# Performance work log

Measured on AMD Instinct MI355X. Metric: run time of the kernel, lower is better.

Reference implementation:

```python
import jax, jax.numpy as jnp
import numpy as np

N, E, R = 50000, 500000, 3
IN, HID, OUT = 128, 128, 128
NEG_SLOPE = 0.2


def setup_inputs() -> dict:
    key = jax.random.key(0)
    ks = jax.random.split(key, 16)
    g = lambda i, shape: jax.random.normal(ks[i], shape, jnp.float32) * 0.1
    return {
        "x": jax.random.normal(ks[0], (N, IN), jnp.float32),
        "edge_index": jax.random.randint(ks[1], (2, E), 0, N, jnp.int32),
        "edge_type": jax.random.randint(ks[2], (E,), 0, R, jnp.int32),
        "edge_attr": jax.random.normal(ks[3], (E, 1), jnp.float32),
        # conv1 params (RGATConv: per-relation weight, q/k/e attention vectors, edge lin, bias)
        "w1": g(4, (R, IN, HID)), "q1": g(5, (HID, 1)), "k1": g(6, (HID, 1)),
        "le1": g(7, (1, HID)), "e1": g(8, (HID, 1)), "b1": jnp.zeros((HID,), jnp.float32),
        # conv2 params
        "w2": g(9, (R, HID, OUT)), "q2": g(10, (OUT, 1)), "k2": g(11, (OUT, 1)),
        "le2": g(12, (1, OUT)), "e2": g(13, (OUT, 1)), "b2": jnp.zeros((OUT,), jnp.float32),
    }


def _rgat_conv(x, src, dst, edge_type, edge_attr, w, q, k, le, e, b):
    """PyG RGATConv: heads=1, dim=1, additive-self-attention, across-relation softmax."""
    n = x.shape[0]
    # Per-relation linear at node level (equiv. to per-edge bmm with w[edge_type])
    xw = jnp.einsum('ni,rio->rno', x, w)            # [R, N, C]
    x_j = xw[edge_type, src]                          # [E, C] transformed source feats
    x_i = xw[edge_type, dst]                          # [E, C] transformed target feats
    # additive attention logits: q(x_i) + k(x_j) + e(lin_edge(edge_attr))
    alpha = x_i @ q + x_j @ k + (edge_attr @ le) @ e  # [E, 1]
    alpha = jax.nn.leaky_relu(alpha, negative_slope=NEG_SLOPE)
    # across-relation softmax over incoming edges of each target node
    amax = jax.ops.segment_max(alpha, dst, num_segments=n)
    amax = jnp.where(jnp.isfinite(amax), amax, 0.0)   # empty segments -> 0
    ex = jnp.exp(alpha - amax[dst])
    denom = jax.ops.segment_sum(ex, dst, num_segments=n)
    alpha = ex / (denom[dst] + 1e-16)
    # weighted scatter-add aggregation, then bias (concat=True, heads=1)
    out = jax.ops.segment_sum(alpha * x_j, dst, num_segments=n)  # [N, C]
    return out + b


def reference(x, edge_index, edge_type, edge_attr,
              w1, q1, k1, le1, e1, b1,
              w2, q2, k2, le2, e2, b2):
    src, dst = edge_index[0], edge_index[1]
    h = jax.nn.relu(_rgat_conv(x, src, dst, edge_type, edge_attr, w1, q1, k1, le1, e1, b1))
    return _rgat_conv(h, src, dst, edge_type, edge_attr, w2, q2, k2, le2, e2, b2)
```

## Files before the change

kernel.cpp:

```cpp
#include <hip/hip_runtime.h>
#include <hip/hip_bf16.h>
#include <math.h>

typedef __bf16 bf16x8 __attribute__((ext_vector_type(8)));
typedef float f32x4 __attribute__((ext_vector_type(4)));

#define CDIM 128

__global__ void sentinel_kernel(float* outf) {
  if (threadIdx.x == 0) outf[0] = 12345.0f;
}

__global__ __launch_bounds__(256) void prep_hist_kernel(
    const float* __restrict__ w1, const float* __restrict__ w2,
    __hip_bfloat16* __restrict__ wt,
    const float* __restrict__ le1, const float* __restrict__ e1,
    const float* __restrict__ le2, const float* __restrict__ e2,
    float* __restrict__ outc, const int* __restrict__ dstv,
    int* __restrict__ deg, int perW, int E) {
  const int b = blockIdx.x;
  const int tid = threadIdx.x;
  if (b < 48) {
    int t = b * 256 + tid;
    if (t >= perW * 2) return;
    const float* w = (t < perW) ? w1 : w2;
    int tt = (t < perW) ? t : t - perW;
    int r = tt >> 11;
    int rem = tt & 2047;
    int kb = rem >> 7;
    int o = rem & 127;
    const float* wr = w + ((size_t)r << 14);
    union { __hip_bfloat16 h[8]; int4 v; } u;
#pragma unroll
    for (int j = 0; j < 8; ++j)
      u.h[j] = __float2bfloat16(wr[(size_t)(kb * 8 + j) * CDIM + o]);
    *reinterpret_cast<int4*>(wt + (size_t)t * 8) = u.v;
  } else if (b == 48) {
    if (tid < 64) {
      float v1 = le1[tid] * e1[tid] + le1[tid + 64] * e1[tid + 64];
      float v2 = le2[tid] * e2[tid] + le2[tid + 64] * e2[tid + 64];
#pragma unroll
      for (int off = 32; off > 0; off >>= 1) {
        v1 += __shfl_xor(v1, off, 64);
        v2 += __shfl_xor(v2, off, 64);
      }
      if (tid == 0) { outc[0] = v1; outc[1] = v2; }
    }
  } else {
    int e0 = (b - 49) * 1024 + tid * 4;
    if (e0 + 3 < E) {
      int4 d4 = *reinterpret_cast<const int4*>(&dstv[e0]);
      atomicAdd(&deg[d4.x], 1);
      atomicAdd(&deg[d4.y], 1);
      atomicAdd(&deg[d4.z], 1);
      atomicAdd(&deg[d4.w], 1);
    } else {
      for (int t = 0; t < 4; ++t) {
        int e = e0 + t;
        if (e < E) atomicAdd(&deg[dstv[e]], 1);
      }
    }
  }
}


__global__ __launch_bounds__(256) void scan1_kernel(const int* __restrict__ deg,
                                                    int* __restrict__ rowptr,
                                                    int* __restrict__ partials, int n) {
  __shared__ int sh[256];
  int t = threadIdx.x;
  int base = blockIdx.x * 1024;
  int idx = base + t * 4;
  int v[4]; int s = 0;
#pragma unroll
  for (int j = 0; j < 4; ++j) { v[j] = (idx + j < n) ? deg[idx + j] : 0; s += v[j]; }
  sh[t] = s;
  __syncthreads();
  for (int off = 1; off < 256; off <<= 1) {
    int x = (t >= off) ? sh[t - off] : 0;
    __syncthreads();
    sh[t] += x;
    __syncthreads();
  }
  int excl = sh[t] - s;
  if (t == 255) partials[blockIdx.x] = sh[255];
  int run = excl;
#pragma unroll
  for (int j = 0; j < 4; ++j) {
    if (idx + j < n) rowptr[idx + j] = run;
    run += v[j];
  }
}

__global__ __launch_bounds__(256) void scan3_kernel(int* __restrict__ rowptr,
                                                    int* __restrict__ cursor,
                                                    const int* __restrict__ partials,
                                                    int nb, int n, int E) {
  __shared__ int spfx[64];
  int t = threadIdx.x;
  if (t < 64) {
    int pv = (t < nb) ? partials[t] : 0;
    int v = pv;
#pragma unroll
    for (int off = 1; off < 64; off <<= 1) {
      int u = __shfl_up(v, off, 64);
      if (t >= off) v += u;
    }
    spfx[t] = v - pv;
  }
  __syncthreads();
  int i = blockIdx.x * 256 + t;
  if (i < n) {
    int v = rowptr[i] + spfx[i >> 10];
    rowptr[i] = v;
    cursor[i] = v;
  } else if (i == n) {
    rowptr[n] = E;
  }
}

__global__ __launch_bounds__(256) void scatter_kernel(
    const int* __restrict__ srcv, const int* __restrict__ dstv,
    const int* __restrict__ etype, const float* __restrict__ eattr,
    int* __restrict__ cursor, int2* __restrict__ kattr, int E, int n) {
  int e0 = blockIdx.x * 1024 + threadIdx.x * 4;
  if (e0 + 3 < E) {
    int4 s4 = *reinterpret_cast<const int4*>(&srcv[e0]);
    int4 d4 = *reinterpret_cast<const int4*>(&dstv[e0]);
    int4 t4 = *reinterpret_cast<const int4*>(&etype[e0]);
    float4 a4 = *reinterpret_cast<const float4*>(&eattr[e0]);
    int p0 = atomicAdd(&cursor[d4.x], 1);
    kattr[p0] = make_int2(t4.x * n + s4.x, __float_as_int(a4.x));
    int p1 = atomicAdd(&cursor[d4.y], 1);
    kattr[p1] = make_int2(t4.y * n + s4.y, __float_as_int(a4.y));
    int p2 = atomicAdd(&cursor[d4.z], 1);
    kattr[p2] = make_int2(t4.z * n + s4.z, __float_as_int(a4.z));
    int p3 = atomicAdd(&cursor[d4.w], 1);
    kattr[p3] = make_int2(t4.w * n + s4.w, __float_as_int(a4.w));
  } else {
    for (int t = 0; t < 4; ++t) {
      int e = e0 + t;
      if (e < E) {
        int p = atomicAdd(&cursor[dstv[e]], 1);
        kattr[p] = make_int2(etype[e] * n + srcv[e], __float_as_int(eattr[e]));
      }
    }
  }
}

template <int BF16IN>
__device__ __forceinline__ void gemm_body64(
    int tb, const float* __restrict__ xf, const __hip_bfloat16* __restrict__ xb,
    const __hip_bfloat16* __restrict__ wt,
    const float* __restrict__ qv, const float* __restrict__ kv,
    __hip_bfloat16* __restrict__ xwout, float* __restrict__ sq,
    float* __restrict__ sk, int n, __hip_bfloat16* wlds, float* qls, float* kls) {
  const int tid = threadIdx.x;
  const int wave = tid >> 6, lane = tid & 63;
  const int quad = lane >> 4, c16 = lane & 15;
  const int m = tb * 64 + wave * 16 + c16;
  const bool ok = m < n;

  if (tid < 128) qls[tid] = qv[tid];
  else kls[tid - 128] = kv[tid - 128];

  bf16x8 zf;
#pragma unroll
  for (int j = 0; j < 8; ++j) zf[j] = (__bf16)0.0f;

  bf16x8 af[4];
#pragma unroll
  for (int ks = 0; ks < 4; ++ks) {
    if (ok) {
      if (BF16IN) {
        af[ks] = *reinterpret_cast<const bf16x8*>(
            xb + (size_t)m * CDIM + ks * 32 + quad * 8);
      } else {
        const float* xp = xf + (size_t)m * CDIM + ks * 32 + quad * 8;
        f32x4 x0 = *reinterpret_cast<const f32x4*>(xp);
        f32x4 x1 = *reinterpret_cast<const f32x4*>(xp + 4);
        bf16x8 a;
#pragma unroll
        for (int j = 0; j < 4; ++j) { a[j] = (__bf16)x0[j]; a[4 + j] = (__bf16)x1[j]; }
        af[ks] = a;
      }
    } else {
      af[ks] = zf;
    }
  }

  for (int r = 0; r < 3; ++r) {
    if (r) __syncthreads();
    {
      const int4* src = reinterpret_cast<const int4*>(wt + ((size_t)r << 14));
      int4* dst = reinterpret_cast<int4*>(wlds);
#pragma unroll
      for (int i = 0; i < 8; ++i) dst[tid + i * 256] = src[tid + i * 256];
    }
    __syncthreads();

    f32x4 acc[8];
#pragma unroll
    for (int ot = 0; ot < 8; ++ot) acc[ot] = (f32x4){0.f, 0.f, 0.f, 0.f};

#pragma unroll
    for (int ks = 0; ks < 4; ++ks) {
#pragma unroll
      for (int ot = 0; ot < 8; ++ot) {
        bf16x8 b = *reinterpret_cast<const bf16x8*>(
            &wlds[(((ks * 4 + quad) * 128) + ot * 16 + c16) * 8]);
        acc[ot] = __builtin_amdgcn_mfma_f32_16x16x32_bf16(b, af[ks], acc[ot], 0, 0, 0);
      }
    }

    __hip_bfloat16* rp = xwout + (((size_t)r * n + m) << 7) + quad * 4;
    float s_q = 0.f, s_k = 0.f;
#pragma unroll
    for (int ot = 0; ot < 8; ++ot) {
      f32x4 a = acc[ot];
      f32x4 q4 = *reinterpret_cast<const f32x4*>(&qls[ot * 16 + quad * 4]);
      f32x4 k4 = *reinterpret_cast<const f32x4*>(&kls[ot * 16 + quad * 4]);
      s_q += a[0] * q4[0] + a[1] * q4[1] + a[2] * q4[2] + a[3] * q4[3];
      s_k += a[0] * k4[0] + a[1] * k4[1] + a[2] * k4[2] + a[3] * k4[3];
      if (ok) {
        union { __hip_bfloat16 b4[4]; uint2 u; } pk;
#pragma unroll
        for (int t = 0; t < 4; ++t) pk.b4[t] = __float2bfloat16(a[t]);
        *reinterpret_cast<uint2*>(rp + ot * 16) = pk.u;
      }
    }
    s_q += __shfl_xor(s_q, 16, 64);
    s_q += __shfl_xor(s_q, 32, 64);
    s_k += __shfl_xor(s_k, 16, 64);
    s_k += __shfl_xor(s_k, 32, 64);
    if (quad == 0 && ok) {
      sq[(size_t)r * n + m] = s_q;
      sk[(size_t)r * n + m] = s_k;
    }
  }
}

__global__ __launch_bounds__(256) void gemm_xw_f32_kernel(
    const float* __restrict__ xin, const __hip_bfloat16* __restrict__ wt,
    const float* __restrict__ qv, const float* __restrict__ kv,
    __hip_bfloat16* __restrict__ xwout, float* __restrict__ sq, float* __restrict__ sk,
    int n) {
  __shared__ __hip_bfloat16 wlds[16 * 128 * 8];
  __shared__ float qls[128], kls[128];
  gemm_body64<0>(blockIdx.x, xin, nullptr, wt, qv, kv, xwout, sq, sk, n,
                 wlds, qls, kls);
}

__global__ __launch_bounds__(256) void gemm_xw_bf16_kernel(
    const __hip_bfloat16* __restrict__ xin, const __hip_bfloat16* __restrict__ wt,
    const float* __restrict__ qv, const float* __restrict__ kv,
    __hip_bfloat16* __restrict__ xwout, float* __restrict__ sq, float* __restrict__ sk,
    int n) {
  __shared__ __hip_bfloat16 wlds[16 * 128 * 8];
  __shared__ float qls[128], kls[128];
  gemm_body64<1>(blockIdx.x, nullptr, xin, wt, qv, kv, xwout, sq, sk, n,
                 wlds, qls, kls);
}

template <int OUTBF16>
__global__ __launch_bounds__(256) void aggregate_kernel(
    const int* __restrict__ rowptr, const int2* __restrict__ kattr,
    const float* __restrict__ sq, const float* __restrict__ sk,
    const __hip_bfloat16* __restrict__ xw, const float* __restrict__ bias,
    const float* __restrict__ cscal, float* __restrict__ outf,
    __hip_bfloat16* __restrict__ outb, int n) {
  const int wave = threadIdx.x >> 6, lane = threadIdx.x & 63;
  const int g = lane >> 4;
  const int sub = lane & 15;
  const int node = blockIdx.x * 16 + wave * 4 + g;
  if (node >= n) return;
  const float c = cscal[0];
  const int n2 = n * 2;

  const int start = rowptr[node];
  const int deg = rowptr[node + 1] - start;
  const float s0 = sq[node], s1 = sq[n + node], s2 = sq[n2 + node];

  float acc[8];
#pragma unroll
  for (int t = 0; t < 8; ++t) acc[t] = 0.f;
  float den = 0.f;

  if (deg > 0) {
    int2 kaA0, kaA1, kaA2, kaA3;
    kaA0 = kattr[start + (0 < deg ? 0 : 0)];
    kaA1 = kattr[start + (1 < deg ? 1 : 0)];
    kaA2 = kattr[start + (2 < deg ? 2 : 0)];
    kaA3 = kattr[start + (3 < deg ? 3 : 0)];
    for (int j0 = 0; j0 < deg; j0 += 4) {
      int nj = j0 + 4;
      int2 kaB0 = kattr[start + (nj + 0 < deg ? nj + 0 : 0)];
      int2 kaB1 = kattr[start + (nj + 1 < deg ? nj + 1 : 0)];
      int2 kaB2 = kattr[start + (nj + 2 < deg ? nj + 2 : 0)];
      int2 kaB3 = kattr[start + (nj + 3 < deg ? nj + 3 : 0)];

      int2 ka[4] = {kaA0, kaA1, kaA2, kaA3};
      float w[4];
      bf16x8 f[4];
#pragma unroll
      for (int t = 0; t < 4; ++t) {
        int kk = ka[t].x;
        float sv = (kk >= n2) ? s2 : ((kk >= n) ? s1 : s0);
        float l = sv + sk[kk] + c * __int_as_float(ka[t].y);
        l = l > 0.f ? l : 0.2f * l;
        w[t] = (j0 + t < deg) ? __expf(l) : 0.f;
        f[t] = *reinterpret_cast<const bf16x8*>(xw + ((size_t)kk << 7) + sub * 8);
      }
#pragma unroll
      for (int t = 0; t < 8; ++t)
        acc[t] += w[0] * (float)f[0][t] + w[1] * (float)f[1][t] +
                  w[2] * (float)f[2][t] + w[3] * (float)f[3][t];
      den += (w[0] + w[1]) + (w[2] + w[3]);

      kaA0 = kaB0; kaA1 = kaB1; kaA2 = kaB2; kaA3 = kaB3;
    }
  }

  float inv = 1.0f / (den + 1e-16f);
  f32x4 b0 = *reinterpret_cast<const f32x4*>(bias + sub * 8);
  f32x4 b1 = *reinterpret_cast<const f32x4*>(bias + sub * 8 + 4);
  f32x4 o0, o1;
#pragma unroll
  for (int t = 0; t < 4; ++t) {
    o0[t] = acc[t] * inv + b0[t];
    o1[t] = acc[4 + t] * inv + b1[t];
  }
  if (OUTBF16) {
    union { __hip_bfloat16 h[8]; int4 v; } pk;
#pragma unroll
    for (int t = 0; t < 4; ++t) {
      pk.h[t] = __float2bfloat16(fmaxf(o0[t], 0.f));
      pk.h[4 + t] = __float2bfloat16(fmaxf(o1[t], 0.f));
    }
    *reinterpret_cast<int4*>(outb + (size_t)node * CDIM + sub * 8) = pk.v;
  } else {
    float* op = outf + (size_t)node * CDIM + sub * 8;
    *reinterpret_cast<f32x4*>(op) = o0;
    *reinterpret_cast<f32x4*>(op + 4) = o1;
  }
}


extern "C" void kernel_launch(void* const* d_in, const int* in_sizes, int n_in,
                              void* d_out, int out_size, void* d_ws, size_t ws_size,
                              hipStream_t stream) {
  const float* x     = (const float*)d_in[0];
  const int*   eidx  = (const int*)d_in[1];
  const int*   etype = (const int*)d_in[2];
  const float* eattr = (const float*)d_in[3];
  const float* w1  = (const float*)d_in[4];
  const float* q1  = (const float*)d_in[5];
  const float* k1  = (const float*)d_in[6];
  const float* le1 = (const float*)d_in[7];
  const float* e1  = (const float*)d_in[8];
  const float* b1  = (const float*)d_in[9];
  const float* w2  = (const float*)d_in[10];
  const float* q2  = (const float*)d_in[11];
  const float* k2  = (const float*)d_in[12];
  const float* le2 = (const float*)d_in[13];
  const float* e2  = (const float*)d_in[14];
  const float* b2  = (const float*)d_in[15];

  const int N = in_sizes[0] / CDIM;
  const int E = in_sizes[2];
  const int R = in_sizes[4] / (CDIM * CDIM);
  const int* srcv = eidx;
  const int* dstv = eidx + E;

  char* p = (char*)d_ws;
  auto alloc = [&](size_t bytes) -> void* {
    void* q = (void*)p;
    p += (bytes + 255) & ~(size_t)255;
    return q;
  };
  float* sq       = (float*)alloc((size_t)R * N * 4);
  float* sk       = (float*)alloc((size_t)R * N * 4);
  int*   deg      = (int*)alloc((size_t)N * 4);
  int*   rowptr   = (int*)alloc((size_t)(N + 1) * 4);
  int*   cursor   = (int*)alloc((size_t)N * 4);
  int*   partials = (int*)alloc(4096);
  int2*  kattr    = (int2*)alloc((size_t)E * 8);
  __hip_bfloat16* wt = (__hip_bfloat16*)alloc((size_t)2 * R * CDIM * CDIM * 2);
  float* cscal    = (float*)alloc(256);
  __hip_bfloat16* xw = (__hip_bfloat16*)alloc((size_t)R * N * CDIM * 2);
  __hip_bfloat16* hb = (__hip_bfloat16*)alloc((size_t)N * CDIM * 2);

  size_t needed = (size_t)(p - (char*)d_ws);
  if (needed > ws_size) {
    sentinel_kernel<<<1, 64, 0, stream>>>((float*)d_out);
    return;
  }

  float* outp = (float*)d_out;

  const int eg4 = (E + 1023) / 1024;
  const int nb = (N + 1023) / 1024;
  const int NT = (N + 63) / 64;
  const int nodes16 = (N + 15) / 16;
  const int perW = R * 2048;

  hipMemsetAsync(deg, 0, (size_t)N * 4, stream);

  prep_hist_kernel<<<49 + eg4, 256, 0, stream>>>(w1, w2, wt, le1, e1, le2, e2,
                                                 cscal, dstv, deg, perW, E);

  scan1_kernel<<<nb, 256, 0, stream>>>(deg, rowptr, partials, N);
  scan3_kernel<<<(N + 1 + 255) / 256, 256, 0, stream>>>(rowptr, cursor, partials, nb, N, E);

  scatter_kernel<<<eg4, 256, 0, stream>>>(srcv, dstv, etype, eattr, cursor, kattr, E, N);

  gemm_xw_f32_kernel<<<NT, 256, 0, stream>>>(x, wt, q1, k1, xw, sq, sk, N);

  aggregate_kernel<1><<<nodes16, 256, 0, stream>>>(rowptr, kattr, sq, sk, xw, b1,
                                                   cscal + 0, nullptr, hb, N);

  gemm_xw_bf16_kernel<<<NT, 256, 0, stream>>>(hb, wt + (size_t)R * CDIM * CDIM,
                                              q2, k2, xw, sq, sk, N);

  aggregate_kernel<0><<<nodes16, 256, 0, stream>>>(rowptr, kattr, sq, sk, xw, b2,
                                                   cscal + 1, outp, nullptr, N);
}
```

Measured before the change: 257.4 us.

## Fuse edge scatter into first GEMM launch, enlarge GEMM tile, simplify aggregate loop

The CSR scatter kernel is merged into the layer-1 GEMM launch as extra blocks, so the independent scatter and GEMM work run concurrently in one launch. Each GEMM block now handles 128 rows instead of 64, with two accumulator sets per wave, which halves how often the weights are reloaded into LDS. The aggregate kernel drops its software-prefetch double-buffering of edge records in favour of a simpler loop. The trade-offs are higher register pressure in the GEMM, fewer GEMM blocks, and possibly less latency hiding in aggregation.

```diff
diff --git a/kernel.cpp b/kernel.cpp
--- a/kernel.cpp
+++ b/kernel.cpp
@@ -119,47 +119,17 @@
   }
 }
 
-__global__ __launch_bounds__(256) void scatter_kernel(
-    const int* __restrict__ srcv, const int* __restrict__ dstv,
-    const int* __restrict__ etype, const float* __restrict__ eattr,
-    int* __restrict__ cursor, int2* __restrict__ kattr, int E, int n) {
-  int e0 = blockIdx.x * 1024 + threadIdx.x * 4;
-  if (e0 + 3 < E) {
-    int4 s4 = *reinterpret_cast<const int4*>(&srcv[e0]);
-    int4 d4 = *reinterpret_cast<const int4*>(&dstv[e0]);
-    int4 t4 = *reinterpret_cast<const int4*>(&etype[e0]);
-    float4 a4 = *reinterpret_cast<const float4*>(&eattr[e0]);
-    int p0 = atomicAdd(&cursor[d4.x], 1);
-    kattr[p0] = make_int2(t4.x * n + s4.x, __float_as_int(a4.x));
-    int p1 = atomicAdd(&cursor[d4.y], 1);
-    kattr[p1] = make_int2(t4.y * n + s4.y, __float_as_int(a4.y));
-    int p2 = atomicAdd(&cursor[d4.z], 1);
-    kattr[p2] = make_int2(t4.z * n + s4.z, __float_as_int(a4.z));
-    int p3 = atomicAdd(&cursor[d4.w], 1);
-    kattr[p3] = make_int2(t4.w * n + s4.w, __float_as_int(a4.w));
-  } else {
-    for (int t = 0; t < 4; ++t) {
-      int e = e0 + t;
-      if (e < E) {
-        int p = atomicAdd(&cursor[dstv[e]], 1);
-        kattr[p] = make_int2(etype[e] * n + srcv[e], __float_as_int(eattr[e]));
-      }
-    }
-  }
-}
-
 template <int BF16IN>
-__device__ __forceinline__ void gemm_body64(
-    int tb, const float* __restrict__ xf, const __hip_bfloat16* __restrict__ xb,
+__device__ __forceinline__ void gemm_body128(
+    int tileb, const float* __restrict__ xf, const __hip_bfloat16* __restrict__ xb,
     const __hip_bfloat16* __restrict__ wt,
     const float* __restrict__ qv, const float* __restrict__ kv,
     __hip_bfloat16* __restrict__ xwout, float* __restrict__ sq,
     float* __restrict__ sk, int n, __hip_bfloat16* wlds, float* qls, float* kls) {
+  const int base = tileb * 128;
   const int tid = threadIdx.x;
   const int wave = tid >> 6, lane = tid & 63;
   const int quad = lane >> 4, c16 = lane & 15;
-  const int m = tb * 64 + wave * 16 + c16;
-  const bool ok = m < n;
 
   if (tid < 128) qls[tid] = qv[tid];
   else kls[tid - 128] = kv[tid - 128];
@@ -168,24 +138,28 @@
 #pragma unroll
   for (int j = 0; j < 8; ++j) zf[j] = (__bf16)0.0f;
 
-  bf16x8 af[4];
-#pragma unroll
-  for (int ks = 0; ks < 4; ++ks) {
-    if (ok) {
-      if (BF16IN) {
-        af[ks] = *reinterpret_cast<const bf16x8*>(
-            xb + (size_t)m * CDIM + ks * 32 + quad * 8);
+  bf16x8 af[2][4];
+#pragma unroll
+  for (int h = 0; h < 2; ++h) {
+    int m = base + wave * 32 + h * 16 + c16;
+#pragma unroll
+    for (int ks = 0; ks < 4; ++ks) {
+      if (m < n) {
+        if (BF16IN) {
+          af[h][ks] = *reinterpret_cast<const bf16x8*>(
+              xb + (size_t)m * CDIM + ks * 32 + quad * 8);
+        } else {
+          const float* xp = xf + (size_t)m * CDIM + ks * 32 + quad * 8;
+          f32x4 x0 = *reinterpret_cast<const f32x4*>(xp);
+          f32x4 x1 = *reinterpret_cast<const f32x4*>(xp + 4);
+          bf16x8 a;
+#pragma unroll
+          for (int j = 0; j < 4; ++j) { a[j] = (__bf16)x0[j]; a[4 + j] = (__bf16)x1[j]; }
+          af[h][ks] = a;
+        }
       } else {
-        const float* xp = xf + (size_t)m * CDIM + ks * 32 + quad * 8;
-        f32x4 x0 = *reinterpret_cast<const f32x4*>(xp);
-        f32x4 x1 = *reinterpret_cast<const f32x4*>(xp + 4);
-        bf16x8 a;
-#pragma unroll
-        for (int j = 0; j < 4; ++j) { a[j] = (__bf16)x0[j]; a[4 + j] = (__bf16)x1[j]; }
-        af[ks] = a;
-      }
-    } else {
-      af[ks] = zf;
+        af[h][ks] = zf;
+      }
     }
   }
 
@@ -199,9 +173,11 @@
     }
     __syncthreads();
 
-    f32x4 acc[8];
-#pragma unroll
-    for (int ot = 0; ot < 8; ++ot) acc[ot] = (f32x4){0.f, 0.f, 0.f, 0.f};
+    f32x4 acc[2][8];
+#pragma unroll
+    for (int h = 0; h < 2; ++h)
+#pragma unroll
+      for (int ot = 0; ot < 8; ++ot) acc[h][ot] = (f32x4){0.f, 0.f, 0.f, 0.f};
 
 #pragma unroll
     for (int ks = 0; ks < 4; ++ks) {
@@ -209,46 +185,81 @@
       for (int ot = 0; ot < 8; ++ot) {
         bf16x8 b = *reinterpret_cast<const bf16x8*>(
             &wlds[(((ks * 4 + quad) * 128) + ot * 16 + c16) * 8]);
-        acc[ot] = __builtin_amdgcn_mfma_f32_16x16x32_bf16(b, af[ks], acc[ot], 0, 0, 0);
-      }
-    }
-
-    __hip_bfloat16* rp = xwout + (((size_t)r * n + m) << 7) + quad * 4;
-    float s_q = 0.f, s_k = 0.f;
-#pragma unroll
-    for (int ot = 0; ot < 8; ++ot) {
-      f32x4 a = acc[ot];
-      f32x4 q4 = *reinterpret_cast<const f32x4*>(&qls[ot * 16 + quad * 4]);
-      f32x4 k4 = *reinterpret_cast<const f32x4*>(&kls[ot * 16 + quad * 4]);
-      s_q += a[0] * q4[0] + a[1] * q4[1] + a[2] * q4[2] + a[3] * q4[3];
-      s_k += a[0] * k4[0] + a[1] * k4[1] + a[2] * k4[2] + a[3] * k4[3];
-      if (ok) {
-        union { __hip_bfloat16 b4[4]; uint2 u; } pk;
-#pragma unroll
-        for (int t = 0; t < 4; ++t) pk.b4[t] = __float2bfloat16(a[t]);
-        *reinterpret_cast<uint2*>(rp + ot * 16) = pk.u;
-      }
-    }
-    s_q += __shfl_xor(s_q, 16, 64);
-    s_q += __shfl_xor(s_q, 32, 64);
-    s_k += __shfl_xor(s_k, 16, 64);
-    s_k += __shfl_xor(s_k, 32, 64);
-    if (quad == 0 && ok) {
-      sq[(size_t)r * n + m] = s_q;
-      sk[(size_t)r * n + m] = s_k;
-    }
-  }
-}
-
-__global__ __launch_bounds__(256) void gemm_xw_f32_kernel(
+        acc[0][ot] = __builtin_amdgcn_mfma_f32_16x16x32_bf16(b, af[0][ks], acc[0][ot], 0, 0, 0);
+        acc[1][ot] = __builtin_amdgcn_mfma_f32_16x16x32_bf16(b, af[1][ks], acc[1][ot], 0, 0, 0);
+      }
+    }
+
+#pragma unroll
+    for (int h = 0; h < 2; ++h) {
+      const int grow = base + wave * 32 + h * 16 + c16;
+      const bool ok = grow < n;
+      __hip_bfloat16* rp = xwout + (((size_t)r * n + grow) << 7) + quad * 4;
+      float s_q = 0.f, s_k = 0.f;
+#pragma unroll
+      for (int ot = 0; ot < 8; ++ot) {
+        f32x4 a = acc[h][ot];
+        f32x4 q4 = *reinterpret_cast<const f32x4*>(&qls[ot * 16 + quad * 4]);
+        f32x4 k4 = *reinterpret_cast<const f32x4*>(&kls[ot * 16 + quad * 4]);
+        s_q += a[0] * q4[0] + a[1] * q4[1] + a[2] * q4[2] + a[3] * q4[3];
+        s_k += a[0] * k4[0] + a[1] * k4[1] + a[2] * k4[2] + a[3] * k4[3];
+        if (ok) {
+          union { __hip_bfloat16 b4[4]; uint2 u; } pk;
+#pragma unroll
+          for (int t = 0; t < 4; ++t) pk.b4[t] = __float2bfloat16(a[t]);
+          *reinterpret_cast<uint2*>(rp + ot * 16) = pk.u;
+        }
+      }
+      s_q += __shfl_xor(s_q, 16, 64);
+      s_q += __shfl_xor(s_q, 32, 64);
+      s_k += __shfl_xor(s_k, 16, 64);
+      s_k += __shfl_xor(s_k, 32, 64);
+      if (quad == 0 && ok) {
+        sq[(size_t)r * n + grow] = s_q;
+        sk[(size_t)r * n + grow] = s_k;
+      }
+    }
+  }
+}
+
+__global__ __launch_bounds__(256) void gemm_scatter_kernel(
     const float* __restrict__ xin, const __hip_bfloat16* __restrict__ wt,
     const float* __restrict__ qv, const float* __restrict__ kv,
     __hip_bfloat16* __restrict__ xwout, float* __restrict__ sq, float* __restrict__ sk,
-    int n) {
+    const int* __restrict__ srcv, const int* __restrict__ dstv,
+    const int* __restrict__ etype, const float* __restrict__ eattr,
+    int* __restrict__ cursor, int2* __restrict__ kattr,
+    int NT, int n, int E) {
   __shared__ __hip_bfloat16 wlds[16 * 128 * 8];
   __shared__ float qls[128], kls[128];
-  gemm_body64<0>(blockIdx.x, xin, nullptr, wt, qv, kv, xwout, sq, sk, n,
-                 wlds, qls, kls);
+  const int b = blockIdx.x;
+  if (b < NT) {
+    gemm_body128<0>(b, xin, nullptr, wt, qv, kv, xwout, sq, sk, n, wlds, qls, kls);
+  } else {
+    int e0 = (b - NT) * 1024 + threadIdx.x * 4;
+    if (e0 + 3 < E) {
+      int4 s4 = *reinterpret_cast<const int4*>(&srcv[e0]);
+      int4 d4 = *reinterpret_cast<const int4*>(&dstv[e0]);
+      int4 t4 = *reinterpret_cast<const int4*>(&etype[e0]);
+      float4 a4 = *reinterpret_cast<const float4*>(&eattr[e0]);
+      int p0 = atomicAdd(&cursor[d4.x], 1);
+      kattr[p0] = make_int2(t4.x * n + s4.x, __float_as_int(a4.x));
+      int p1 = atomicAdd(&cursor[d4.y], 1);
+      kattr[p1] = make_int2(t4.y * n + s4.y, __float_as_int(a4.y));
+      int p2 = atomicAdd(&cursor[d4.z], 1);
+      kattr[p2] = make_int2(t4.z * n + s4.z, __float_as_int(a4.z));
+      int p3 = atomicAdd(&cursor[d4.w], 1);
+      kattr[p3] = make_int2(t4.w * n + s4.w, __float_as_int(a4.w));
+    } else {
+      for (int t = 0; t < 4; ++t) {
+        int e = e0 + t;
+        if (e < E) {
+          int p = atomicAdd(&cursor[dstv[e]], 1);
+          kattr[p] = make_int2(etype[e] * n + srcv[e], __float_as_int(eattr[e]));
+        }
+      }
+    }
+  }
 }
 
 __global__ __launch_bounds__(256) void gemm_xw_bf16_kernel(
@@ -258,8 +269,8 @@
     int n) {
   __shared__ __hip_bfloat16 wlds[16 * 128 * 8];
   __shared__ float qls[128], kls[128];
-  gemm_body64<1>(blockIdx.x, nullptr, xin, wt, qv, kv, xwout, sq, sk, n,
-                 wlds, qls, kls);
+  gemm_body128<1>(blockIdx.x, nullptr, xin, wt, qv, kv, xwout, sq, sk, n,
+                  wlds, qls, kls);
 }
 
 template <int OUTBF16>
@@ -286,39 +297,29 @@
   for (int t = 0; t < 8; ++t) acc[t] = 0.f;
   float den = 0.f;
 
-  if (deg > 0) {
-    int2 kaA0, kaA1, kaA2, kaA3;
-    kaA0 = kattr[start + (0 < deg ? 0 : 0)];
-    kaA1 = kattr[start + (1 < deg ? 1 : 0)];
-    kaA2 = kattr[start + (2 < deg ? 2 : 0)];
-    kaA3 = kattr[start + (3 < deg ? 3 : 0)];
-    for (int j0 = 0; j0 < deg; j0 += 4) {
-      int nj = j0 + 4;
-      int2 kaB0 = kattr[start + (nj + 0 < deg ? nj + 0 : 0)];
-      int2 kaB1 = kattr[start + (nj + 1 < deg ? nj + 1 : 0)];
-      int2 kaB2 = kattr[start + (nj + 2 < deg ? nj + 2 : 0)];
-      int2 kaB3 = kattr[start + (nj + 3 < deg ? nj + 3 : 0)];
-
-      int2 ka[4] = {kaA0, kaA1, kaA2, kaA3};
-      float w[4];
-      bf16x8 f[4];
-#pragma unroll
-      for (int t = 0; t < 4; ++t) {
-        int kk = ka[t].x;
-        float sv = (kk >= n2) ? s2 : ((kk >= n) ? s1 : s0);
-        float l = sv + sk[kk] + c * __int_as_float(ka[t].y);
-        l = l > 0.f ? l : 0.2f * l;
-        w[t] = (j0 + t < deg) ? __expf(l) : 0.f;
-        f[t] = *reinterpret_cast<const bf16x8*>(xw + ((size_t)kk << 7) + sub * 8);
-      }
-#pragma unroll
-      for (int t = 0; t < 8; ++t)
-        acc[t] += w[0] * (float)f[0][t] + w[1] * (float)f[1][t] +
-                  w[2] * (float)f[2][t] + w[3] * (float)f[3][t];
-      den += (w[0] + w[1]) + (w[2] + w[3]);
-
-      kaA0 = kaB0; kaA1 = kaB1; kaA2 = kaB2; kaA3 = kaB3;
-    }
+  for (int j0 = 0; j0 < deg; j0 += 4) {
+    int2 ka[4];
+#pragma unroll
+    for (int t = 0; t < 4; ++t) {
+      int idx = j0 + t;
+      ka[t] = kattr[start + (idx < deg ? idx : 0)];
+    }
+    float w[4];
+    bf16x8 f[4];
+#pragma unroll
+    for (int t = 0; t < 4; ++t) {
+      int kk = ka[t].x;
+      float sv = (kk >= n2) ? s2 : ((kk >= n) ? s1 : s0);
+      float l = sv + sk[kk] + c * __int_as_float(ka[t].y);
+      l = l > 0.f ? l : 0.2f * l;
+      w[t] = (j0 + t < deg) ? __expf(l) : 0.f;
+      f[t] = *reinterpret_cast<const bf16x8*>(xw + ((size_t)kk << 7) + sub * 8);
+    }
+#pragma unroll
+    for (int t = 0; t < 8; ++t)
+      acc[t] += w[0] * (float)f[0][t] + w[1] * (float)f[1][t] +
+                w[2] * (float)f[2][t] + w[3] * (float)f[3][t];
+    den += (w[0] + w[1]) + (w[2] + w[3]);
   }
 
   float inv = 1.0f / (den + 1e-16f);
@@ -400,7 +401,7 @@
 
   const int eg4 = (E + 1023) / 1024;
   const int nb = (N + 1023) / 1024;
-  const int NT = (N + 63) / 64;
+  const int NT = (N + 127) / 128;
   const int nodes16 = (N + 15) / 16;
   const int perW = R * 2048;
 
@@ -412,9 +413,9 @@
   scan1_kernel<<<nb, 256, 0, stream>>>(deg, rowptr, partials, N);
   scan3_kernel<<<(N + 1 + 255) / 256, 256, 0, stream>>>(rowptr, cursor, partials, nb, N, E);
 
-  scatter_kernel<<<eg4, 256, 0, stream>>>(srcv, dstv, etype, eattr, cursor, kattr, E, N);
-
-  gemm_xw_f32_kernel<<<NT, 256, 0, stream>>>(x, wt, q1, k1, xw, sq, sk, N);
+  gemm_scatter_kernel<<<NT + eg4, 256, 0, stream>>>(x, wt, q1, k1, xw, sq, sk,
+                                                    srcv, dstv, etype, eattr,
+                                                    cursor, kattr, NT, N, E);
 
   aggregate_kernel<1><<<nodes16, 256, 0, stream>>>(rowptr, kattr, sq, sk, xw, b1,
                                                    cscal + 0, nullptr, hb, N);
```

Result: faster. 239.8 us (-6.8%).
